# Kernel tuning notes

Measured on AMD Instinct MI355X. Metric: run time of the kernel, lower is better.

The kernel has to match this reference:

```python
import jax, jax.numpy as jnp
import numpy as np

N = 50000          # nodes
E = 800000         # edges
IN = 256           # input feature dim
HID = 64           # hidden per-head dim
OUT = 64           # output dim
H1, H2 = 4, 1      # heads per layer
NEG_SLOPE = 0.2    # DGL GATConv default


def setup_inputs() -> dict:
    key = jax.random.key(0)
    ks = jax.random.split(key, 12)
    features = jax.random.normal(ks[0], (N, IN), dtype=jnp.float32)
    src = jax.random.randint(ks[1], (E,), 0, N, dtype=jnp.int32)
    dst = jax.random.randint(ks[2], (E,), 0, N, dtype=jnp.int32)
    s1 = 1.0 / np.sqrt(IN)
    s2 = 1.0 / np.sqrt(HID * H1)
    W1 = jax.random.normal(ks[3], (IN, H1 * HID), dtype=jnp.float32) * s1
    al1 = jax.random.normal(ks[4], (H1, HID), dtype=jnp.float32) * 0.1
    ar1 = jax.random.normal(ks[5], (H1, HID), dtype=jnp.float32) * 0.1
    b1 = jnp.zeros((H1, HID), dtype=jnp.float32)
    W2 = jax.random.normal(ks[6], (H1 * HID, H2 * OUT), dtype=jnp.float32) * s2
    al2 = jax.random.normal(ks[7], (H2, OUT), dtype=jnp.float32) * 0.1
    ar2 = jax.random.normal(ks[8], (H2, OUT), dtype=jnp.float32) * 0.1
    b2 = jnp.zeros((H2, OUT), dtype=jnp.float32)
    return {"features": features, "src": src, "dst": dst,
            "W1": W1, "al1": al1, "ar1": ar1, "b1": b1,
            "W2": W2, "al2": al2, "ar2": ar2, "b2": b2}


def gat_layer(h, src, dst, W, al, ar, b, heads, out_dim, activate):
    # projection: (N, H, D)
    feat = (h @ W).reshape(N, heads, out_dim)
    # per-node attention halves: (N, H)
    el = jnp.einsum('nhd,hd->nh', feat, al)
    er = jnp.einsum('nhd,hd->nh', feat, ar)
    # edge logits with leaky relu: (E, H)
    e = el[src] + er[dst]
    e = jnp.where(e >= 0, e, NEG_SLOPE * e)
    # edge softmax grouped by destination node
    emax = jax.ops.segment_max(e, dst, num_segments=N)      # (N, H)
    ee = jnp.exp(e - emax[dst])
    esum = jax.ops.segment_sum(ee, dst, num_segments=N)     # (N, H)
    alpha = ee / esum[dst]                                  # (E, H)
    # weighted scatter-sum of source features: (N, H, D)
    msg = alpha[:, :, None] * feat[src]
    out = jax.ops.segment_sum(msg, dst, num_segments=N) + b[None]
    if activate:
        out = jax.nn.relu(out)
    return out


def reference(features, src, dst, W1, al1, ar1, b1, W2, al2, ar2, b2):
    h = gat_layer(features, src, dst, W1, al1, ar1, b1, H1, HID, True)
    h = h.reshape(N, H1 * HID)                 # flatten(1)
    h = gat_layer(h, src, dst, W2, al2, ar2, b2, H2, OUT, False)
    return h.mean(axis=1)                      # mean over heads -> (N, OUT)
```

## Files before the change

kernel.cpp:

```cpp
#include <hip/hip_runtime.h>
#include <hip/hip_fp16.h>

#define NN   50000
#define NE   800000
#define IND  256
#define HIDD 64
#define OUTD 64
#define NH1  4
#define NH2  1
#define NEG  0.2f

#define NBUK 196
#define NCHK 256
#define CE   3125
#define MAXDEG 96

typedef float f32x4 __attribute__((ext_vector_type(4)));
typedef short s16x8 __attribute__((ext_vector_type(8)));

__device__ __forceinline__ short bf16_rne(float f) {
    unsigned u = __float_as_uint(f);
    unsigned r = u + 0x7FFFu + ((u >> 16) & 1u);
    return (short)(r >> 16);
}

__global__ void cnt1a_k(const int* __restrict__ key, int* __restrict__ cnt) {
    __shared__ int lc[NBUK];
    int tid = threadIdx.x, chunk = blockIdx.x;
    for (int j = tid; j < NBUK; j += 256) lc[j] = 0;
    __syncthreads();
    const int* kc = key + (size_t)chunk * CE;
    for (int t = tid; t < CE; t += 256) atomicAdd(&lc[kc[t] >> 8], 1);
    __syncthreads();
    for (int j = tid; j < NBUK; j += 256) cnt[j * NCHK + chunk] = lc[j];
}

__global__ void cnt1b_k(const int2* __restrict__ ein, int* __restrict__ cnt) {
    __shared__ int lc[NBUK];
    int tid = threadIdx.x, chunk = blockIdx.x;
    for (int j = tid; j < NBUK; j += 256) lc[j] = 0;
    __syncthreads();
    const int2* ec = ein + (size_t)chunk * CE;
    for (int t = tid; t < CE; t += 256) atomicAdd(&lc[ec[t].y >> 8], 1);
    __syncthreads();
    for (int j = tid; j < NBUK; j += 256) cnt[j * NCHK + chunk] = lc[j];
}

__global__ void scanC_k(int* __restrict__ cnt, int* __restrict__ buktot) {
    int b    = blockIdx.x * 4 + (threadIdx.x >> 6);
    int lane = threadIdx.x & 63;
    if (b >= NBUK) return;
    int base = b * NCHK + lane * 4;
    int4 v = *(int4*)&cnt[base];
    int s0 = v.x, s1 = s0 + v.y, s2 = s1 + v.z, s3 = s2 + v.w;
    int inc = s3;
    for (int o = 1; o < 64; o <<= 1) {
        int t = __shfl_up(inc, o);
        if (lane >= o) inc += t;
    }
    int excl = inc - s3;
    int4 w;
    w.x = excl; w.y = excl + s0; w.z = excl + s1; w.w = excl + s2;
    *(int4*)&cnt[base] = w;
    if (lane == 63) buktot[b] = inc;
}

__global__ void fill1a_k(const int* __restrict__ src, const int* __restrict__ dst,
                         const int* __restrict__ cnt, const int* __restrict__ buktot,
                         int2* __restrict__ eout) {
    __shared__ int cur[NBUK];
    __shared__ int tmp[256];
    int tid = threadIdx.x, chunk = blockIdx.x;
    int v = (tid < NBUK) ? buktot[tid] : 0;
    tmp[tid] = v;
    __syncthreads();
    for (int o = 1; o < 256; o <<= 1) {
        int add = (tid >= o) ? tmp[tid - o] : 0;
        __syncthreads();
        tmp[tid] += add;
        __syncthreads();
    }
    if (tid < NBUK) cur[tid] = cnt[tid * NCHK + chunk] + tmp[tid] - v;
    __syncthreads();
    size_t base = (size_t)chunk * CE;
    for (int t = tid; t < CE; t += 256) {
        int s = src[base + t], d = dst[base + t];
        int pos = atomicAdd(&cur[s >> 8], 1);
        eout[pos] = make_int2(s, d);
    }
}

__global__ void fill1b_k(const int2* __restrict__ ein, const int* __restrict__ cnt,
                         const int* __restrict__ buktot, int2* __restrict__ eout) {
    __shared__ int cur[NBUK];
    __shared__ int tmp[256];
    int tid = threadIdx.x, chunk = blockIdx.x;
    int v = (tid < NBUK) ? buktot[tid] : 0;
    tmp[tid] = v;
    __syncthreads();
    for (int o = 1; o < 256; o <<= 1) {
        int add = (tid >= o) ? tmp[tid - o] : 0;
        __syncthreads();
        tmp[tid] += add;
        __syncthreads();
    }
    if (tid < NBUK) cur[tid] = cnt[tid * NCHK + chunk] + tmp[tid] - v;
    __syncthreads();
    const int2* ec = ein + (size_t)chunk * CE;
    for (int t = tid; t < CE; t += 256) {
        int2 e = ec[t];
        int pos = atomicAdd(&cur[e.y >> 8], 1);
        eout[pos] = e;
    }
}

__global__ void fill2_k(const int2* __restrict__ ein, const int* __restrict__ buktot,
                        int* __restrict__ off, int* __restrict__ deg,
                        int* __restrict__ src_sorted) {
    __shared__ int lh[256];
    __shared__ int tmp[256];
    __shared__ int cur[256];
    int tid = threadIdx.x, b = blockIdx.x;
    int v0 = (tid < NBUK) ? buktot[tid] : 0;
    tmp[tid] = v0;
    __syncthreads();
    for (int o = 1; o < 256; o <<= 1) {
        int add = (tid >= o) ? tmp[tid - o] : 0;
        __syncthreads();
        tmp[tid] += add;
        __syncthreads();
    }
    int beg = (b > 0) ? tmp[b - 1] : 0;
    int end = tmp[b];
    __syncthreads();
    int node0 = b << 8;
    lh[tid] = 0;
    __syncthreads();
    for (int e = beg + tid; e < end; e += 256)
        atomicAdd(&lh[ein[e].y - node0], 1);
    __syncthreads();
    int v = lh[tid];
    tmp[tid] = v;
    __syncthreads();
    for (int o = 1; o < 256; o <<= 1) {
        int add = (tid >= o) ? tmp[tid - o] : 0;
        __syncthreads();
        tmp[tid] += add;
        __syncthreads();
    }
    int excl = tmp[tid] - v;
    int node = node0 + tid;
    if (node < NN) { deg[node] = v; off[node] = beg + excl; }
    cur[tid] = excl;
    __syncthreads();
    for (int e = beg + tid; e < end; e += 256) {
        int2 ed = ein[e];
        int r = atomicAdd(&cur[ed.y - node0], 1);
        src_sorted[beg + r] = ed.x;
    }
}

__global__ void wsplitT_k(const float* __restrict__ W1, const float* __restrict__ W2,
                          short* __restrict__ Wh1, short* __restrict__ Wh2) {
    int idx = blockIdx.x * 256 + threadIdx.x;
    if (idx < IND * IND) {
        int k = idx / IND, n = idx - k * IND;
        Wh1[(size_t)n * IND + k] = bf16_rne(W1[idx]);
    } else if (idx < IND * IND + IND * OUTD) {
        int i2 = idx - IND * IND;
        int k = i2 / OUTD, n = i2 - k * OUTD;
        Wh2[(size_t)n * IND + k] = bf16_rne(W2[i2]);
    }
}

__global__ __launch_bounds__(256) void gemm_l1(const float* __restrict__ A,
                                               const short* __restrict__ Bt,
                                               const float* __restrict__ al,
                                               const float* __restrict__ ar,
                                               __half* __restrict__ C,
                                               float* __restrict__ el,
                                               float* __restrict__ er, int M) {
    const int K = 256;
    __shared__ short As[64][40];
    __shared__ short Bs[256][40];

    int tid  = threadIdx.x;
    int wid  = tid >> 6, lane = tid & 63;
    int wm   = (wid >> 1) * 32;
    int wn   = (wid & 1) * 128;
    int row0 = blockIdx.x * 64;

    int arow = tid >> 2;
    int aseg = (tid & 3) * 8;
    int mr   = lane & 15;
    int kg   = (lane >> 4) * 8;

    f32x4 acc[2][8];
#pragma unroll
    for (int i = 0; i < 2; ++i)
#pragma unroll
        for (int j = 0; j < 8; ++j) acc[i][j] = (f32x4)(0.f);

    for (int k0 = 0; k0 < K; k0 += 32) {
        {
            int r = row0 + arow;
            float v[8];
            if (r < M) {
                float4 f0 = *(const float4*)&A[(size_t)r * K + k0 + aseg];
                float4 f1 = *(const float4*)&A[(size_t)r * K + k0 + aseg + 4];
                v[0] = f0.x; v[1] = f0.y; v[2] = f0.z; v[3] = f0.w;
                v[4] = f1.x; v[5] = f1.y; v[6] = f1.z; v[7] = f1.w;
            } else {
#pragma unroll
                for (int q = 0; q < 8; ++q) v[q] = 0.f;
            }
            short hi[8];
#pragma unroll
            for (int q = 0; q < 8; ++q) hi[q] = bf16_rne(v[q]);
            *(s16x8*)&As[arow][aseg] = *(s16x8*)&hi[0];
        }
        {
#pragma unroll
            for (int rep = 0; rep < 4; ++rep) {
                int n = rep * 64 + (tid >> 2);
                int ks = (tid & 3) * 8;
                *(s16x8*)&Bs[n][ks] = *(const s16x8*)&Bt[(size_t)n * K + k0 + ks];
            }
        }
        __syncthreads();

        s16x8 ah[2];
#pragma unroll
        for (int mi = 0; mi < 2; ++mi)
            ah[mi] = *(const s16x8*)&As[wm + mi * 16 + mr][kg];
#pragma unroll
        for (int ni = 0; ni < 8; ++ni) {
            s16x8 bhv = *(const s16x8*)&Bs[wn + ni * 16 + mr][kg];
#pragma unroll
            for (int mi = 0; mi < 2; ++mi)
                acc[mi][ni] = __builtin_amdgcn_mfma_f32_16x16x32_bf16(ah[mi], bhv, acc[mi][ni], 0, 0, 0);
        }
        __syncthreads();
    }

    float av[8], rv[8];
#pragma unroll
    for (int ni = 0; ni < 8; ++ni) {
        int c = wn + ni * 16 + mr;
        av[ni] = al[c];
        rv[ni] = ar[c];
    }
    int h0 = wn >> 6;

#pragma unroll
    for (int mi = 0; mi < 2; ++mi) {
#pragma unroll
        for (int r4 = 0; r4 < 4; ++r4) {
            int rr = row0 + wm + mi * 16 + (lane >> 4) * 4 + r4;
            if (rr < M) {
#pragma unroll
                for (int ni = 0; ni < 8; ++ni)
                    C[(size_t)rr * 256 + wn + ni * 16 + mr] = __float2half(acc[mi][ni][r4]);
            }
            float e0 = 0.f, e1 = 0.f, f0 = 0.f, f1 = 0.f;
#pragma unroll
            for (int ni = 0; ni < 4; ++ni) {
                e0 += acc[mi][ni][r4] * av[ni];
                f0 += acc[mi][ni][r4] * rv[ni];
            }
#pragma unroll
            for (int ni = 4; ni < 8; ++ni) {
                e1 += acc[mi][ni][r4] * av[ni];
                f1 += acc[mi][ni][r4] * rv[ni];
            }
#pragma unroll
            for (int o = 1; o <= 8; o <<= 1) {
                e0 += __shfl_xor(e0, o); e1 += __shfl_xor(e1, o);
                f0 += __shfl_xor(f0, o); f1 += __shfl_xor(f1, o);
            }
            if (mr == 0 && rr < M) {
                el[rr * 4 + h0]     = e0;
                el[rr * 4 + h0 + 1] = e1;
                er[rr * 4 + h0]     = f0;
                er[rr * 4 + h0 + 1] = f1;
            }
        }
    }
}

__global__ __launch_bounds__(256) void gemm_l2(const short* __restrict__ A,
                                               const short* __restrict__ Bt,
                                               const float* __restrict__ al,
                                               const float* __restrict__ ar,
                                               __half* __restrict__ C,
                                               float* __restrict__ el,
                                               float* __restrict__ er, int M) {
    const int K = 256;
    __shared__ short As[128][40];
    __shared__ short Bs[64][40];

    int tid  = threadIdx.x;
    int wid  = tid >> 6, lane = tid & 63;
    int wm   = wid * 32;
    int row0 = blockIdx.x * 128;

    int arow = tid >> 1;
    int aseg = (tid & 1) * 16;
    int mr   = lane & 15;
    int kg   = (lane >> 4) * 8;

    f32x4 acc[2][4];
#pragma unroll
    for (int i = 0; i < 2; ++i)
#pragma unroll
        for (int j = 0; j < 4; ++j) acc[i][j] = (f32x4)(0.f);

    for (int k0 = 0; k0 < K; k0 += 32) {
        {
            int r = row0 + arow;
            if (r < M) {
                *(s16x8*)&As[arow][aseg]     = *(const s16x8*)&A[(size_t)r * K + k0 + aseg];
                *(s16x8*)&As[arow][aseg + 8] = *(const s16x8*)&A[(size_t)r * K + k0 + aseg + 8];
            } else {
                s16x8 z = (s16x8)(short)0;
                *(s16x8*)&As[arow][aseg]     = z;
                *(s16x8*)&As[arow][aseg + 8] = z;
            }
        }
        {
            int n  = tid >> 2;
            int ks = (tid & 3) * 8;
            *(s16x8*)&Bs[n][ks] = *(const s16x8*)&Bt[(size_t)n * K + k0 + ks];
        }
        __syncthreads();

        s16x8 av_[2];
#pragma unroll
        for (int mi = 0; mi < 2; ++mi)
            av_[mi] = *(const s16x8*)&As[wm + mi * 16 + mr][kg];
#pragma unroll
        for (int ni = 0; ni < 4; ++ni) {
            s16x8 bhv = *(const s16x8*)&Bs[ni * 16 + mr][kg];
#pragma unroll
            for (int mi = 0; mi < 2; ++mi)
                acc[mi][ni] = __builtin_amdgcn_mfma_f32_16x16x32_bf16(av_[mi], bhv, acc[mi][ni], 0, 0, 0);
        }
        __syncthreads();
    }

    float av[4], rv[4];
#pragma unroll
    for (int ni = 0; ni < 4; ++ni) {
        int c = ni * 16 + mr;
        av[ni] = al[c];
        rv[ni] = ar[c];
    }

#pragma unroll
    for (int mi = 0; mi < 2; ++mi) {
#pragma unroll
        for (int r4 = 0; r4 < 4; ++r4) {
            int rr = row0 + wm + mi * 16 + (lane >> 4) * 4 + r4;
            if (rr < M) {
#pragma unroll
                for (int ni = 0; ni < 4; ++ni)
                    C[(size_t)rr * 64 + ni * 16 + mr] = __float2half(acc[mi][ni][r4]);
            }
            float e0 = 0.f, f0 = 0.f;
#pragma unroll
            for (int ni = 0; ni < 4; ++ni) {
                e0 += acc[mi][ni][r4] * av[ni];
                f0 += acc[mi][ni][r4] * rv[ni];
            }
#pragma unroll
            for (int o = 1; o <= 8; o <<= 1) {
                e0 += __shfl_xor(e0, o);
                f0 += __shfl_xor(f0, o);
            }
            if (mr == 0 && rr < M) { el[rr] = e0; er[rr] = f0; }
        }
    }
}

__global__ void agg_sm_l1(const __half* __restrict__ feat, const float* __restrict__ el,
                          const float* __restrict__ er, const int* __restrict__ src_sorted,
                          const int* __restrict__ off, const int* __restrict__ deg,
                          const float* __restrict__ bias, short* __restrict__ out) {
    __shared__ float alds[4][MAXDEG * 4];
    int w    = threadIdx.x >> 6;
    int wid  = blockIdx.x * 4 + w;
    int lane = threadIdx.x & 63;
    if (wid >= NN) return;
    int e   = lane >> 5;
    int c8  = (lane & 31) * 8;
    int h   = (lane & 31) >> 3;
    int k   = lane & 7;
    int sub = e * 8 + k;
    int beg = off[wid], dg = deg[wid];
    float erdh = er[(size_t)wid * 4 + h];

    float sum = 0.f;
    for (int p = sub; p < dg; p += 16) {
        int s = src_sorted[beg + p];
        float x = el[(size_t)s * 4 + h] + erdh;
        x = (x >= 0.f) ? x : NEG * x;
        float ex = __expf(x);
        if (p < MAXDEG) alds[w][p * 4 + h] = ex;
        sum += ex;
    }
    sum += __shfl_xor(sum, 1);
    sum += __shfl_xor(sum, 2);
    sum += __shfl_xor(sum, 4);
    sum += __shfl_xor(sum, 32);
    float inv = (dg > 0) ? 1.f / sum : 0.f;

    float acc[8] = {};
    int p = e;
    for (; p + 2 < dg; p += 4) {
        int s0 = src_sorted[beg + p];
        int s1 = src_sorted[beg + p + 2];
        float a0, a1;
        if (p < MAXDEG) a0 = alds[w][p * 4 + h];
        else {
            float x = el[(size_t)s0 * 4 + h] + erdh;
            x = (x >= 0.f) ? x : NEG * x;
            a0 = __expf(x);
        }
        if (p + 2 < MAXDEG) a1 = alds[w][(p + 2) * 4 + h];
        else {
            float x = el[(size_t)s1 * 4 + h] + erdh;
            x = (x >= 0.f) ? x : NEG * x;
            a1 = __expf(x);
        }
        float4 r0 = *(const float4*)&feat[(size_t)s0 * 256 + c8];
        float4 r1 = *(const float4*)&feat[(size_t)s1 * 256 + c8];
        __half2* h0 = (__half2*)&r0;
        __half2* h1 = (__half2*)&r1;
#pragma unroll
        for (int q = 0; q < 4; ++q) {
            float2 f0 = __half22float2(h0[q]);
            float2 f1 = __half22float2(h1[q]);
            acc[2 * q]     += a0 * f0.x + a1 * f1.x;
            acc[2 * q + 1] += a0 * f0.y + a1 * f1.y;
        }
    }
    for (; p < dg; p += 2) {
        int s = src_sorted[beg + p];
        float a;
        if (p < MAXDEG) a = alds[w][p * 4 + h];
        else {
            float x = el[(size_t)s * 4 + h] + erdh;
            x = (x >= 0.f) ? x : NEG * x;
            a = __expf(x);
        }
        float4 raw = *(const float4*)&feat[(size_t)s * 256 + c8];
        __half2* hh = (__half2*)&raw;
#pragma unroll
        for (int q = 0; q < 4; ++q) {
            float2 f = __half22float2(hh[q]);
            acc[2 * q]     += a * f.x;
            acc[2 * q + 1] += a * f.y;
        }
    }
#pragma unroll
    for (int q = 0; q < 8; ++q) acc[q] += __shfl_xor(acc[q], 32);
    if (e == 0) {
        short ob[8];
#pragma unroll
        for (int q = 0; q < 8; ++q) {
            float v = fmaxf(acc[q] * inv + bias[c8 + q], 0.f);
            ob[q] = bf16_rne(v);
        }
        *(s16x8*)&out[(size_t)wid * 256 + c8] = *(s16x8*)&ob[0];
    }
}

__global__ void agg_sm_l2(const __half* __restrict__ feat, const float* __restrict__ el,
                          const float* __restrict__ er, const int* __restrict__ src_sorted,
                          const int* __restrict__ off, const int* __restrict__ deg,
                          const float* __restrict__ bias, float* __restrict__ out) {
    __shared__ float alds[4][MAXDEG];
    int w    = threadIdx.x >> 6;
    int wid  = blockIdx.x * 4 + w;
    int lane = threadIdx.x & 63;
    if (wid >= NN) return;
    int e   = lane >> 3;
    int c8  = (lane & 7) * 8;
    int beg = off[wid], dg = deg[wid];
    float erd = er[wid];

    float sum = 0.f;
    for (int p = lane; p < dg; p += 64) {
        int s = src_sorted[beg + p];
        float x = el[s] + erd;
        x = (x >= 0.f) ? x : NEG * x;
        float ex = __expf(x);
        if (p < MAXDEG) alds[w][p] = ex;
        sum += ex;
    }
#pragma unroll
    for (int o = 1; o <= 32; o <<= 1) sum += __shfl_xor(sum, o);
    float inv = (dg > 0) ? 1.f / sum : 0.f;

    float acc[8] = {};
    for (int p = 0; p < dg; p += 8) {
        if (p + e < dg) {
            int s = src_sorted[beg + p + e];
            float a;
            if (p + e < MAXDEG) a = alds[w][p + e];
            else {
                float x = el[s] + erd;
                x = (x >= 0.f) ? x : NEG * x;
                a = __expf(x);
            }
            float4 raw = *(const float4*)&feat[(size_t)s * 64 + c8];
            __half2* hh = (__half2*)&raw;
#pragma unroll
            for (int q = 0; q < 4; ++q) {
                float2 f = __half22float2(hh[q]);
                acc[2 * q]     += a * f.x;
                acc[2 * q + 1] += a * f.y;
            }
        }
    }
#pragma unroll
    for (int o = 8; o <= 32; o <<= 1)
#pragma unroll
        for (int q = 0; q < 8; ++q) acc[q] += __shfl_xor(acc[q], o);
    if (e == 0) {
        float4 b0 = *(const float4*)&bias[c8];
        float4 b1 = *(const float4*)&bias[c8 + 4];
        float4 o0 = make_float4(acc[0] * inv + b0.x, acc[1] * inv + b0.y,
                                acc[2] * inv + b0.z, acc[3] * inv + b0.w);
        float4 o1 = make_float4(acc[4] * inv + b1.x, acc[5] * inv + b1.y,
                                acc[6] * inv + b1.z, acc[7] * inv + b1.w);
        *(float4*)&out[(size_t)wid * 64 + c8]     = o0;
        *(float4*)&out[(size_t)wid * 64 + c8 + 4] = o1;
    }
}

extern "C" void kernel_launch(void* const* d_in, const int* in_sizes, int n_in,
                              void* d_out, int out_size, void* d_ws, size_t ws_size,
                              hipStream_t stream) {
    const float* features = (const float*)d_in[0];
    const int*   src      = (const int*)  d_in[1];
    const int*   dst      = (const int*)  d_in[2];
    const float* W1       = (const float*)d_in[3];
    const float* al1      = (const float*)d_in[4];
    const float* ar1      = (const float*)d_in[5];
    const float* b1       = (const float*)d_in[6];
    const float* W2       = (const float*)d_in[7];
    const float* al2      = (const float*)d_in[8];
    const float* ar2      = (const float*)d_in[9];
    const float* b2       = (const float*)d_in[10];
    float* out = (float*)d_out;

    char* base = (char*)d_ws;
    size_t o = 0;
    __half* feat1h = (__half*)(base + o); o += (size_t)NN * 256 * 2;
    short*  h1b    = (short*) (base + o); o += (size_t)NN * 256 * 2;
    float*  el1 = (float*)(base + o); o += (size_t)NN * 4 * 4;
    float*  er1 = (float*)(base + o); o += (size_t)NN * 4 * 4;
    float*  el2 = (float*)(base + o); o += (size_t)NN * 4;
    float*  er2 = (float*)(base + o); o += (size_t)NN * 4;
    int* deg        = (int*)(base + o); o += (size_t)NN * 4;
    int* off        = (int*)(base + o); o += (size_t)NN * 4;
    int* src_sorted = (int*)(base + o); o += (size_t)NE * 4;
    int* cnt        = (int*)(base + o); o += (size_t)NBUK * NCHK * 4;
    int* buktot     = (int*)(base + o); o += 1024;
    int2* ebufS = (int2*)(base + o); o += (size_t)NE * 8;
    int2* ebufD = (int2*)(base + o); o += (size_t)NE * 8;
    short* Wt1 = (short*)(base + o); o += (size_t)IND * IND * 2;
    short* Wt2 = (short*)(base + o); o += (size_t)OUTD * IND * 2;

    __half* feat2h = feat1h;

    cnt1a_k<<<NCHK, 256, 0, stream>>>(src, cnt);
    scanC_k<<<(NBUK + 3) / 4, 256, 0, stream>>>(cnt, buktot);
    fill1a_k<<<NCHK, 256, 0, stream>>>(src, dst, cnt, buktot, ebufS);
    cnt1b_k<<<NCHK, 256, 0, stream>>>(ebufS, cnt);
    scanC_k<<<(NBUK + 3) / 4, 256, 0, stream>>>(cnt, buktot);
    fill1b_k<<<NCHK, 256, 0, stream>>>(ebufS, cnt, buktot, ebufD);
    fill2_k<<<NBUK, 256, 0, stream>>>(ebufD, buktot, off, deg, src_sorted);

    wsplitT_k<<<(IND * IND + IND * OUTD + 255) / 256, 256, 0, stream>>>(W1, W2, Wt1, Wt2);

    gemm_l1<<<(NN + 63) / 64, 256, 0, stream>>>(features, Wt1, al1, ar1,
                                                feat1h, el1, er1, NN);
    agg_sm_l1<<<(NN + 3) / 4, 256, 0, stream>>>(feat1h, el1, er1, src_sorted, off, deg,
                                                b1, h1b);

    gemm_l2<<<(NN + 127) / 128, 256, 0, stream>>>(h1b, Wt2, al2, ar2,
                                                  feat2h, el2, er2, NN);
    agg_sm_l2<<<(NN + 3) / 4, 256, 0, stream>>>(feat2h, el2, er2, src_sorted, off, deg,
                                                b2, out);
}
```

Before: 185.3 us.

## Fuse graph-sort preprocessing and weight transpose into one cooperative kernel

Replaces the seven-kernel counting-sort chain and the weight bf16 transpose with a single cooperative kernel of 256 blocks, using grid-wide syncs between phases. The goal is to remove per-launch overhead and inter-kernel gaps across many small kernels. In exchange, grid.sync barriers add their own cost. The final per-bucket phase uses only 196 of the 256 blocks, so some occupancy is lost.

```diff
diff --git a/kernel.cpp b/kernel.cpp
--- a/kernel.cpp
+++ b/kernel.cpp
@@ -1,5 +1,8 @@
 #include <hip/hip_runtime.h>
 #include <hip/hip_fp16.h>
+#include <hip/hip_cooperative_groups.h>
+
+namespace cg = cooperative_groups;
 
 #define NN   50000
 #define NE   800000
@@ -24,152 +27,172 @@
     return (short)(r >> 16);
 }
 
-__global__ void cnt1a_k(const int* __restrict__ key, int* __restrict__ cnt) {
-    __shared__ int lc[NBUK];
-    int tid = threadIdx.x, chunk = blockIdx.x;
-    for (int j = tid; j < NBUK; j += 256) lc[j] = 0;
-    __syncthreads();
-    const int* kc = key + (size_t)chunk * CE;
-    for (int t = tid; t < CE; t += 256) atomicAdd(&lc[kc[t] >> 8], 1);
-    __syncthreads();
-    for (int j = tid; j < NBUK; j += 256) cnt[j * NCHK + chunk] = lc[j];
-}
-
-__global__ void cnt1b_k(const int2* __restrict__ ein, int* __restrict__ cnt) {
-    __shared__ int lc[NBUK];
-    int tid = threadIdx.x, chunk = blockIdx.x;
-    for (int j = tid; j < NBUK; j += 256) lc[j] = 0;
-    __syncthreads();
-    const int2* ec = ein + (size_t)chunk * CE;
-    for (int t = tid; t < CE; t += 256) atomicAdd(&lc[ec[t].y >> 8], 1);
-    __syncthreads();
-    for (int j = tid; j < NBUK; j += 256) cnt[j * NCHK + chunk] = lc[j];
-}
-
-__global__ void scanC_k(int* __restrict__ cnt, int* __restrict__ buktot) {
-    int b    = blockIdx.x * 4 + (threadIdx.x >> 6);
-    int lane = threadIdx.x & 63;
-    if (b >= NBUK) return;
-    int base = b * NCHK + lane * 4;
-    int4 v = *(int4*)&cnt[base];
-    int s0 = v.x, s1 = s0 + v.y, s2 = s1 + v.z, s3 = s2 + v.w;
-    int inc = s3;
-    for (int o = 1; o < 64; o <<= 1) {
-        int t = __shfl_up(inc, o);
-        if (lane >= o) inc += t;
-    }
-    int excl = inc - s3;
-    int4 w;
-    w.x = excl; w.y = excl + s0; w.z = excl + s1; w.w = excl + s2;
-    *(int4*)&cnt[base] = w;
-    if (lane == 63) buktot[b] = inc;
-}
-
-__global__ void fill1a_k(const int* __restrict__ src, const int* __restrict__ dst,
-                         const int* __restrict__ cnt, const int* __restrict__ buktot,
-                         int2* __restrict__ eout) {
-    __shared__ int cur[NBUK];
-    __shared__ int tmp[256];
-    int tid = threadIdx.x, chunk = blockIdx.x;
-    int v = (tid < NBUK) ? buktot[tid] : 0;
-    tmp[tid] = v;
-    __syncthreads();
-    for (int o = 1; o < 256; o <<= 1) {
-        int add = (tid >= o) ? tmp[tid - o] : 0;
-        __syncthreads();
-        tmp[tid] += add;
-        __syncthreads();
-    }
-    if (tid < NBUK) cur[tid] = cnt[tid * NCHK + chunk] + tmp[tid] - v;
-    __syncthreads();
-    size_t base = (size_t)chunk * CE;
-    for (int t = tid; t < CE; t += 256) {
-        int s = src[base + t], d = dst[base + t];
-        int pos = atomicAdd(&cur[s >> 8], 1);
-        eout[pos] = make_int2(s, d);
-    }
-}
-
-__global__ void fill1b_k(const int2* __restrict__ ein, const int* __restrict__ cnt,
-                         const int* __restrict__ buktot, int2* __restrict__ eout) {
-    __shared__ int cur[NBUK];
-    __shared__ int tmp[256];
-    int tid = threadIdx.x, chunk = blockIdx.x;
-    int v = (tid < NBUK) ? buktot[tid] : 0;
-    tmp[tid] = v;
-    __syncthreads();
-    for (int o = 1; o < 256; o <<= 1) {
-        int add = (tid >= o) ? tmp[tid - o] : 0;
-        __syncthreads();
-        tmp[tid] += add;
-        __syncthreads();
-    }
-    if (tid < NBUK) cur[tid] = cnt[tid * NCHK + chunk] + tmp[tid] - v;
-    __syncthreads();
-    const int2* ec = ein + (size_t)chunk * CE;
-    for (int t = tid; t < CE; t += 256) {
-        int2 e = ec[t];
-        int pos = atomicAdd(&cur[e.y >> 8], 1);
-        eout[pos] = e;
-    }
-}
-
-__global__ void fill2_k(const int2* __restrict__ ein, const int* __restrict__ buktot,
-                        int* __restrict__ off, int* __restrict__ deg,
-                        int* __restrict__ src_sorted) {
+__global__ void build_coop(const int* __restrict__ src, const int* __restrict__ dst,
+                           const float* __restrict__ W1, const float* __restrict__ W2,
+                           short* __restrict__ Wt1, short* __restrict__ Wt2,
+                           int* __restrict__ cnt, int* __restrict__ buktot,
+                           int2* __restrict__ ebufS, int2* __restrict__ ebufD,
+                           int* __restrict__ off, int* __restrict__ deg,
+                           int* __restrict__ src_sorted) {
+    cg::grid_group grid = cg::this_grid();
     __shared__ int lh[256];
     __shared__ int tmp[256];
     __shared__ int cur[256];
-    int tid = threadIdx.x, b = blockIdx.x;
-    int v0 = (tid < NBUK) ? buktot[tid] : 0;
-    tmp[tid] = v0;
+    int tid = threadIdx.x, blk = blockIdx.x;
+
+    for (int idx = blk * 256 + tid; idx < IND * IND + IND * OUTD; idx += 256 * 256) {
+        if (idx < IND * IND) {
+            int k = idx / IND, n = idx - k * IND;
+            Wt1[(size_t)n * IND + k] = bf16_rne(W1[idx]);
+        } else {
+            int i2 = idx - IND * IND;
+            int k = i2 / OUTD, n = i2 - k * OUTD;
+            Wt2[(size_t)n * IND + k] = bf16_rne(W2[i2]);
+        }
+    }
+
+    for (int j = tid; j < NBUK; j += 256) lh[j] = 0;
     __syncthreads();
-    for (int o = 1; o < 256; o <<= 1) {
-        int add = (tid >= o) ? tmp[tid - o] : 0;
-        __syncthreads();
-        tmp[tid] += add;
-        __syncthreads();
-    }
-    int beg = (b > 0) ? tmp[b - 1] : 0;
-    int end = tmp[b];
+    {
+        const int* kc = src + (size_t)blk * CE;
+        for (int t = tid; t < CE; t += 256) atomicAdd(&lh[kc[t] >> 8], 1);
+    }
     __syncthreads();
-    int node0 = b << 8;
-    lh[tid] = 0;
+    for (int j = tid; j < NBUK; j += 256) cnt[j * NCHK + blk] = lh[j];
+    grid.sync();
+
+    if (blk < (NBUK + 3) / 4) {
+        int b    = blk * 4 + (tid >> 6);
+        int lane = tid & 63;
+        if (b < NBUK) {
+            int base = b * NCHK + lane * 4;
+            int4 v = *(int4*)&cnt[base];
+            int s0 = v.x, s1 = s0 + v.y, s2 = s1 + v.z, s3 = s2 + v.w;
+            int inc = s3;
+            for (int o = 1; o < 64; o <<= 1) {
+                int t = __shfl_up(inc, o);
+                if (lane >= o) inc += t;
+            }
+            int excl = inc - s3;
+            int4 w;
+            w.x = excl; w.y = excl + s0; w.z = excl + s1; w.w = excl + s2;
+            *(int4*)&cnt[base] = w;
+            if (lane == 63) buktot[b] = inc;
+        }
+    }
+    grid.sync();
+
+    {
+        int v = (tid < NBUK) ? buktot[tid] : 0;
+        tmp[tid] = v;
+        __syncthreads();
+        for (int o = 1; o < 256; o <<= 1) {
+            int add = (tid >= o) ? tmp[tid - o] : 0;
+            __syncthreads();
+            tmp[tid] += add;
+            __syncthreads();
+        }
+        if (tid < NBUK) cur[tid] = cnt[tid * NCHK + blk] + tmp[tid] - v;
+        __syncthreads();
+        size_t base = (size_t)blk * CE;
+        for (int t = tid; t < CE; t += 256) {
+            int s = src[base + t], d = dst[base + t];
+            int pos = atomicAdd(&cur[s >> 8], 1);
+            ebufS[pos] = make_int2(s, d);
+        }
+    }
+    grid.sync();
+
+    for (int j = tid; j < NBUK; j += 256) lh[j] = 0;
     __syncthreads();
-    for (int e = beg + tid; e < end; e += 256)
-        atomicAdd(&lh[ein[e].y - node0], 1);
+    {
+        const int2* ec = ebufS + (size_t)blk * CE;
+        for (int t = tid; t < CE; t += 256) atomicAdd(&lh[ec[t].y >> 8], 1);
+    }
     __syncthreads();
-    int v = lh[tid];
-    tmp[tid] = v;
-    __syncthreads();
-    for (int o = 1; o < 256; o <<= 1) {
-        int add = (tid >= o) ? tmp[tid - o] : 0;
-        __syncthreads();
-        tmp[tid] += add;
-        __syncthreads();
-    }
-    int excl = tmp[tid] - v;
-    int node = node0 + tid;
-    if (node < NN) { deg[node] = v; off[node] = beg + excl; }
-    cur[tid] = excl;
-    __syncthreads();
-    for (int e = beg + tid; e < end; e += 256) {
-        int2 ed = ein[e];
-        int r = atomicAdd(&cur[ed.y - node0], 1);
-        src_sorted[beg + r] = ed.x;
-    }
-}
-
-__global__ void wsplitT_k(const float* __restrict__ W1, const float* __restrict__ W2,
-                          short* __restrict__ Wh1, short* __restrict__ Wh2) {
-    int idx = blockIdx.x * 256 + threadIdx.x;
-    if (idx < IND * IND) {
-        int k = idx / IND, n = idx - k * IND;
-        Wh1[(size_t)n * IND + k] = bf16_rne(W1[idx]);
-    } else if (idx < IND * IND + IND * OUTD) {
-        int i2 = idx - IND * IND;
-        int k = i2 / OUTD, n = i2 - k * OUTD;
-        Wh2[(size_t)n * IND + k] = bf16_rne(W2[i2]);
+    for (int j = tid; j < NBUK; j += 256) cnt[j * NCHK + blk] = lh[j];
+    grid.sync();
+
+    if (blk < (NBUK + 3) / 4) {
+        int b    = blk * 4 + (tid >> 6);
+        int lane = tid & 63;
+        if (b < NBUK) {
+            int base = b * NCHK + lane * 4;
+            int4 v = *(int4*)&cnt[base];
+            int s0 = v.x, s1 = s0 + v.y, s2 = s1 + v.z, s3 = s2 + v.w;
+            int inc = s3;
+            for (int o = 1; o < 64; o <<= 1) {
+                int t = __shfl_up(inc, o);
+                if (lane >= o) inc += t;
+            }
+            int excl = inc - s3;
+            int4 w;
+            w.x = excl; w.y = excl + s0; w.z = excl + s1; w.w = excl + s2;
+            *(int4*)&cnt[base] = w;
+            if (lane == 63) buktot[b] = inc;
+        }
+    }
+    grid.sync();
+
+    {
+        int v = (tid < NBUK) ? buktot[tid] : 0;
+        tmp[tid] = v;
+        __syncthreads();
+        for (int o = 1; o < 256; o <<= 1) {
+            int add = (tid >= o) ? tmp[tid - o] : 0;
+            __syncthreads();
+            tmp[tid] += add;
+            __syncthreads();
+        }
+        if (tid < NBUK) cur[tid] = cnt[tid * NCHK + blk] + tmp[tid] - v;
+        __syncthreads();
+        const int2* ec = ebufS + (size_t)blk * CE;
+        for (int t = tid; t < CE; t += 256) {
+            int2 e = ec[t];
+            int pos = atomicAdd(&cur[e.y >> 8], 1);
+            ebufD[pos] = e;
+        }
+    }
+    grid.sync();
+
+    if (blk < NBUK) {
+        int v0 = (tid < NBUK) ? buktot[tid] : 0;
+        tmp[tid] = v0;
+        __syncthreads();
+        for (int o = 1; o < 256; o <<= 1) {
+            int add = (tid >= o) ? tmp[tid - o] : 0;
+            __syncthreads();
+            tmp[tid] += add;
+            __syncthreads();
+        }
+        int beg = (blk > 0) ? tmp[blk - 1] : 0;
+        int end = tmp[blk];
+        __syncthreads();
+        int node0 = blk << 8;
+        lh[tid] = 0;
+        __syncthreads();
+        for (int e = beg + tid; e < end; e += 256)
+            atomicAdd(&lh[ebufD[e].y - node0], 1);
+        __syncthreads();
+        int v = lh[tid];
+        tmp[tid] = v;
+        __syncthreads();
+        for (int o = 1; o < 256; o <<= 1) {
+            int add = (tid >= o) ? tmp[tid - o] : 0;
+            __syncthreads();
+            tmp[tid] += add;
+            __syncthreads();
+        }
+        int excl = tmp[tid] - v;
+        int node = node0 + tid;
+        if (node < NN) { deg[node] = v; off[node] = beg + excl; }
+        cur[tid] = excl;
+        __syncthreads();
+        for (int e = beg + tid; e < end; e += 256) {
+            int2 ed = ebufD[e];
+            int r = atomicAdd(&cur[ed.y - node0], 1);
+            src_sorted[beg + r] = ed.x;
+        }
     }
 }
 
@@ -575,15 +598,16 @@
 
     __half* feat2h = feat1h;
 
-    cnt1a_k<<<NCHK, 256, 0, stream>>>(src, cnt);
-    scanC_k<<<(NBUK + 3) / 4, 256, 0, stream>>>(cnt, buktot);
-    fill1a_k<<<NCHK, 256, 0, stream>>>(src, dst, cnt, buktot, ebufS);
-    cnt1b_k<<<NCHK, 256, 0, stream>>>(ebufS, cnt);
-    scanC_k<<<(NBUK + 3) / 4, 256, 0, stream>>>(cnt, buktot);
-    fill1b_k<<<NCHK, 256, 0, stream>>>(ebufS, cnt, buktot, ebufD);
-    fill2_k<<<NBUK, 256, 0, stream>>>(ebufD, buktot, off, deg, src_sorted);
-
-    wsplitT_k<<<(IND * IND + IND * OUTD + 255) / 256, 256, 0, stream>>>(W1, W2, Wt1, Wt2);
+    {
+        void* args[] = {
+            (void*)&src, (void*)&dst, (void*)&W1, (void*)&W2,
+            (void*)&Wt1, (void*)&Wt2, (void*)&cnt, (void*)&buktot,
+            (void*)&ebufS, (void*)&ebufD, (void*)&off, (void*)&deg,
+            (void*)&src_sorted
+        };
+        hipLaunchCooperativeKernel((const void*)build_coop, dim3(NCHK), dim3(256),
+                                   args, 0, stream);
+    }
 
     gemm_l1<<<(NN + 63) / 64, 256, 0, stream>>>(features, Wt1, al1, ar1,
                                                 feat1h, el1, er1, NN);
```

Measured after the change: 374.6 us. +102.2%, slower.
